# Kernel tuning notes

Measured on AMD Instinct MI355X. Metric: run time of the kernel, lower is better.

The kernel has to match this reference:

```python
import jax, jax.numpy as jnp
import numpy as np

INPUT_SIZE = 1024
NUM_QUBITS = 12
EMBED_SIZE = 2 ** NUM_QUBITS  # 4096
BATCH = 4096


def setup_inputs() -> dict:
    key = jax.random.key(0)
    k_x, k_w, k_p = jax.random.split(key, 3)
    x = jax.random.normal(k_x, (BATCH, INPUT_SIZE), dtype=jnp.float32)
    quantum_weights = jax.random.normal(k_w, (INPUT_SIZE, EMBED_SIZE), dtype=jnp.float32)
    quantum_phases = jax.random.normal(k_p, (INPUT_SIZE, NUM_QUBITS), dtype=jnp.float32)
    return {"x": x, "quantum_weights": quantum_weights, "quantum_phases": quantum_phases}


def reference(x, quantum_weights, quantum_phases):
    # Original: out[b] = Re( sum_j exp(i * mean(phases[j]) * x[b,j]) * W[j,:] ).
    # W is real, so the real part is sum_j cos(mean(phases[j]) * x[b,j]) * W[j,:],
    # i.e. a cosine-modulated matmul.
    phase_mean = jnp.mean(quantum_phases, axis=1)          # [input_size]
    coef = jnp.cos(x * phase_mean[None, :])                # [batch, input_size]
    return coef @ quantum_weights                          # [batch, embed_size]
```

## Files before the change

kernel.cpp:

```cpp
#include <hip/hip_runtime.h>
#include <hip/hip_bf16.h>


#define K_DIM 1024
#define N_DIM 4096
#define B_DIM 4096
#define NQ 12

typedef __attribute__((ext_vector_type(8))) _Float16 f16x8;
typedef __attribute__((ext_vector_type(4))) float f32x4;


__global__ void pm_kernel(const float* __restrict__ phases, float* __restrict__ pm) {
    int j = blockIdx.x * 256 + threadIdx.x;
    if (j < K_DIM) {
        float s = 0.f;
#pragma unroll
        for (int q = 0; q < NQ; ++q) s += phases[j * NQ + q];
        pm[j] = s * (1.0f / NQ);
    }
}

__global__ void asplit_kernel(const float* __restrict__ x, const float* __restrict__ pm,
                              char* __restrict__ Ah) {
    int i = blockIdx.x * 256 + threadIdx.x;
    int row = i >> 7;
    int k0  = (i & 127) << 3;
    const float* xp = x + ((size_t)row << 10) + k0;
    float4 xa = *(const float4*)xp;
    float4 xb = *(const float4*)(xp + 4);
    float4 pa = *(const float4*)(pm + k0);
    float4 pb = *(const float4*)(pm + k0 + 4);
    f16x8 hv;
    hv[0] = (_Float16)__cosf(xa.x * pa.x); hv[1] = (_Float16)__cosf(xa.y * pa.y);
    hv[2] = (_Float16)__cosf(xa.z * pa.z); hv[3] = (_Float16)__cosf(xa.w * pa.w);
    hv[4] = (_Float16)__cosf(xb.x * pb.x); hv[5] = (_Float16)__cosf(xb.y * pb.y);
    hv[6] = (_Float16)__cosf(xb.z * pb.z); hv[7] = (_Float16)__cosf(xb.w * pb.w);
    int tm = row >> 8, kt = k0 >> 5;
    int r = row & 255, kk = k0 & 31;
    size_t base = ((size_t)tm * 32 + (size_t)kt) * 16384;
    int addr = ((r << 6) + (kk << 1)) ^ ((r & 7) << 4);
    *(f16x8*)(Ah + base + addr) = hv;
}

__global__ void wsplit_kernel(const float* __restrict__ W, char* __restrict__ Bf) {
    __shared__ float t[64][65];
    int n0 = blockIdx.x * 64, k0 = blockIdx.y * 64;
    int tid = threadIdx.x;
#pragma unroll
    for (int p = 0; p < 16; ++p) {
        int lin = p * 256 + tid;
        int kk = lin >> 6, nn = lin & 63;
        t[kk][nn] = W[(size_t)(k0 + kk) * N_DIM + n0 + nn];
    }
    __syncthreads();
    int tn = n0 >> 8;
#pragma unroll
    for (int p2 = 0; p2 < 2; ++p2) {
        int w = p2 * 256 + tid;
        int nn = w >> 3, oct = w & 7;
        int r = (n0 & 255) + nn;
        int kt = (k0 >> 5) + (oct >> 2);
        int kk = (oct & 3) * 8;
        f16x8 hv;
#pragma unroll
        for (int j = 0; j < 8; ++j) hv[j] = (_Float16)t[oct * 8 + j][nn];
        size_t base = ((size_t)tn * 32 + (size_t)kt) * 16384;
        int addr = ((r << 6) + (kk << 1)) ^ ((r & 7) << 4);
        *(f16x8*)(Bf + base + addr) = hv;
    }
}

#define GLL16(g, l)                                                           \
    __builtin_amdgcn_global_load_lds(                                         \
        (const __attribute__((address_space(1))) void*)(g),                   \
        (__attribute__((address_space(3))) void*)(l), 16, 0, 0)

__global__ __launch_bounds__(512, 2) void gemm_kernel(
        const char* __restrict__ Ah, const char* __restrict__ Bf,
        float* __restrict__ C) {
    __shared__ char lds[98304];
    const int tid  = threadIdx.x;
    const int lane = tid & 63;
    const int wid  = tid >> 6;
    const int wm = wid >> 2, wn = wid & 3;
    const int fr   = lane & 15;
    const int colb = (lane >> 4) << 4;

    int wg  = blockIdx.x;
    int swz = (wg & 7) * 32 + (wg >> 3);
    int by = swz >> 4, bx = swz & 15;

    const char* pA = Ah + (size_t)by * 32 * 16384;
    const char* pB = Bf + (size_t)bx * 32 * 16384;

    int aAddr[8], bAddr[4];
#pragma unroll
    for (int m = 0; m < 8; ++m) {
        int r = wm * 128 + m * 16 + fr;
        aAddr[m] = ((r << 6) + colb) ^ ((r & 7) << 4);
    }
#pragma unroll
    for (int n = 0; n < 4; ++n) {
        int r = wn * 64 + n * 16 + fr;
        bAddr[n] = ((r << 6) + colb) ^ ((r & 7) << 4);
    }

    const int so = tid << 4;

#pragma unroll
    for (int t = 0; t < 2; ++t) {
        char* d = lds + t * 32768;
        const char* sA = pA + t * 16384;
        const char* sB = pB + t * 16384;
        GLL16(sA + so, d + so);
        GLL16(sA + 8192 + so, d + 8192 + so);
        GLL16(sB + so, d + 16384 + so);
        GLL16(sB + 8192 + so, d + 24576 + so);
    }

    f32x4 acc[8][4];
#pragma unroll
    for (int m = 0; m < 8; ++m)
#pragma unroll
        for (int n = 0; n < 4; ++n)
            acc[m][n] = (f32x4){0.f, 0.f, 0.f, 0.f};

    for (int t = 0; t < 32; ++t) {
        asm volatile("s_waitcnt vmcnt(4)" ::: "memory");
        __builtin_amdgcn_s_barrier();
        __builtin_amdgcn_sched_barrier(0);

        int t2 = (t + 2) & 31;
        char* d2 = lds + ((t + 2) % 3) * 32768;
        const char* sA = pA + t2 * 16384;
        const char* sB = pB + t2 * 16384;
        GLL16(sA + so, d2 + so);
        GLL16(sA + 8192 + so, d2 + 8192 + so);
        GLL16(sB + so, d2 + 16384 + so);
        GLL16(sB + 8192 + so, d2 + 24576 + so);

        const char* bufA = lds + (t % 3) * 32768;
        const char* bufB = bufA + 16384;
        f16x8 aH[8], bF[4];
#pragma unroll
        for (int m = 0; m < 8; ++m) aH[m] = *(const f16x8*)(bufA + aAddr[m]);
#pragma unroll
        for (int n = 0; n < 4; ++n) bF[n] = *(const f16x8*)(bufB + bAddr[n]);

        __builtin_amdgcn_s_setprio(1);
#pragma unroll
        for (int m = 0; m < 8; ++m)
#pragma unroll
            for (int n = 0; n < 4; ++n)
                acc[m][n] = __builtin_amdgcn_mfma_f32_16x16x32_f16(aH[m], bF[n], acc[m][n], 0, 0, 0);
        __builtin_amdgcn_s_setprio(0);
    }

    const int crow0 = by * 256 + wm * 128 + ((lane >> 4) << 2);
    const int ccol0 = bx * 256 + wn * 64 + fr;
#pragma unroll
    for (int m = 0; m < 8; ++m)
#pragma unroll
        for (int n = 0; n < 4; ++n) {
            size_t base = (size_t)(crow0 + m * 16) * N_DIM + (size_t)(ccol0 + n * 16);
#pragma unroll
            for (int j = 0; j < 4; ++j)
                C[base + (size_t)j * N_DIM] = acc[m][n][j];
        }
}

extern "C" void kernel_launch(void* const* d_in, const int* in_sizes, int n_in,
                              void* d_out, int out_size, void* d_ws, size_t ws_size,
                              hipStream_t stream) {
    const float* x      = (const float*)d_in[0];
    const float* W      = (const float*)d_in[1];
    const float* phases = (const float*)d_in[2];
    float* out = (float*)d_out;

    char* ws = (char*)d_ws;
    float* pm = (float*)ws;
    char* Ah = ws + 65536;
    char* Bf = Ah + (size_t)8 * 1024 * 1024;

    pm_kernel<<<4, 256, 0, stream>>>(phases, pm);
    asplit_kernel<<<(B_DIM * (K_DIM / 8)) / 256, 256, 0, stream>>>(x, pm, Ah);
    wsplit_kernel<<<dim3(N_DIM / 64, K_DIM / 64), 256, 0, stream>>>(W, Bf);
    gemm_kernel<<<256, 512, 0, stream>>>(Ah, Bf, out);
}
```

Baseline: 135.1 us.

## Switch GEMM to 64-deep K tiles with interleaved double-buffered loads

Repacks the fp16 A and B operands into 32 KB tiles holding 64 K-values each, two 32-wide halves per tile. The GEMM main loop now runs 16 iterations over a 128 KB LDS double buffer instead of 32 iterations over a 96 KB triple buffer. Async global-to-LDS loads for the next tile are split into four chunks and interleaved with the MFMA sub-blocks of the current tile. The goal is fewer loop iterations and better overlap of memory traffic with matrix math, in exchange for more barriers per iteration and higher LDS use per block.

Result: faster. 131.9 us (-2.4%).

```diff
diff --git a/kernel.cpp b/kernel.cpp
--- a/kernel.cpp
+++ b/kernel.cpp
@@ -36,9 +36,9 @@
     hv[2] = (_Float16)__cosf(xa.z * pa.z); hv[3] = (_Float16)__cosf(xa.w * pa.w);
     hv[4] = (_Float16)__cosf(xb.x * pb.x); hv[5] = (_Float16)__cosf(xb.y * pb.y);
     hv[6] = (_Float16)__cosf(xb.z * pb.z); hv[7] = (_Float16)__cosf(xb.w * pb.w);
-    int tm = row >> 8, kt = k0 >> 5;
+    int tr = row >> 8, kt = k0 >> 6, khalf = (k0 & 63) >> 5;
     int r = row & 255, kk = k0 & 31;
-    size_t base = ((size_t)tm * 32 + (size_t)kt) * 16384;
+    size_t base = ((size_t)tr * 16 + (size_t)kt) * 32768 + (size_t)khalf * 16384;
     int addr = ((r << 6) + (kk << 1)) ^ ((r & 7) << 4);
     *(f16x8*)(Ah + base + addr) = hv;
 }
@@ -54,20 +54,20 @@
         t[kk][nn] = W[(size_t)(k0 + kk) * N_DIM + n0 + nn];
     }
     __syncthreads();
-    int tn = n0 >> 8;
+    int tr = n0 >> 8, kt = k0 >> 6;
+    size_t tbase = ((size_t)tr * 16 + (size_t)kt) * 32768;
 #pragma unroll
     for (int p2 = 0; p2 < 2; ++p2) {
         int w = p2 * 256 + tid;
         int nn = w >> 3, oct = w & 7;
         int r = (n0 & 255) + nn;
-        int kt = (k0 >> 5) + (oct >> 2);
+        int khalf = oct >> 2;
         int kk = (oct & 3) * 8;
         f16x8 hv;
 #pragma unroll
         for (int j = 0; j < 8; ++j) hv[j] = (_Float16)t[oct * 8 + j][nn];
-        size_t base = ((size_t)tn * 32 + (size_t)kt) * 16384;
         int addr = ((r << 6) + (kk << 1)) ^ ((r & 7) << 4);
-        *(f16x8*)(Bf + base + addr) = hv;
+        *(f16x8*)(Bf + tbase + (size_t)khalf * 16384 + addr) = hv;
     }
 }
 
@@ -79,7 +79,7 @@
 __global__ __launch_bounds__(512, 2) void gemm_kernel(
         const char* __restrict__ Ah, const char* __restrict__ Bf,
         float* __restrict__ C) {
-    __shared__ char lds[98304];
+    __shared__ char lds[131072];
     const int tid  = threadIdx.x;
     const int lane = tid & 63;
     const int wid  = tid >> 6;
@@ -89,35 +89,34 @@
 
     int wg  = blockIdx.x;
     int swz = (wg & 7) * 32 + (wg >> 3);
-    int by = swz >> 4, bx = swz & 15;
-
-    const char* pA = Ah + (size_t)by * 32 * 16384;
-    const char* pB = Bf + (size_t)bx * 32 * 16384;
-
-    int aAddr[8], bAddr[4];
+    const int by = swz >> 4, bx = swz & 15;
+
+    const char* pA = Ah + (size_t)by * 16 * 32768;
+    const char* pB = Bf + (size_t)bx * 16 * 32768;
+
+    int aOff[8], bOff[4];
 #pragma unroll
     for (int m = 0; m < 8; ++m) {
         int r = wm * 128 + m * 16 + fr;
-        aAddr[m] = ((r << 6) + colb) ^ ((r & 7) << 4);
+        aOff[m] = ((r << 6) + colb) ^ ((r & 7) << 4);
     }
 #pragma unroll
     for (int n = 0; n < 4; ++n) {
         int r = wn * 64 + n * 16 + fr;
-        bAddr[n] = ((r << 6) + colb) ^ ((r & 7) << 4);
+        bOff[n] = ((r << 6) + colb) ^ ((r & 7) << 4);
     }
 
     const int so = tid << 4;
 
 #pragma unroll
-    for (int t = 0; t < 2; ++t) {
-        char* d = lds + t * 32768;
-        const char* sA = pA + t * 16384;
-        const char* sB = pB + t * 16384;
-        GLL16(sA + so, d + so);
-        GLL16(sA + 8192 + so, d + 8192 + so);
-        GLL16(sB + so, d + 16384 + so);
-        GLL16(sB + 8192 + so, d + 24576 + so);
-    }
+    for (int c = 0; c < 4; ++c) {
+        const char* s = ((c & 1) ? pB : pA) + (c >> 1) * 16384;
+        char* d = lds + c * 16384;
+        GLL16(s + so, d + so);
+        GLL16(s + 8192 + so, d + 8192 + so);
+    }
+    asm volatile("s_waitcnt vmcnt(4)" ::: "memory");
+    __builtin_amdgcn_s_barrier();
 
     f32x4 acc[8][4];
 #pragma unroll
@@ -126,35 +125,53 @@
         for (int n = 0; n < 4; ++n)
             acc[m][n] = (f32x4){0.f, 0.f, 0.f, 0.f};
 
-    for (int t = 0; t < 32; ++t) {
-        asm volatile("s_waitcnt vmcnt(4)" ::: "memory");
-        __builtin_amdgcn_s_barrier();
-        __builtin_amdgcn_sched_barrier(0);
-
-        int t2 = (t + 2) & 31;
-        char* d2 = lds + ((t + 2) % 3) * 32768;
-        const char* sA = pA + t2 * 16384;
-        const char* sB = pB + t2 * 16384;
-        GLL16(sA + so, d2 + so);
-        GLL16(sA + 8192 + so, d2 + 8192 + so);
-        GLL16(sB + so, d2 + 16384 + so);
-        GLL16(sB + 8192 + so, d2 + 24576 + so);
-
-        const char* bufA = lds + (t % 3) * 32768;
-        const char* bufB = bufA + 16384;
-        f16x8 aH[8], bF[4];
-#pragma unroll
-        for (int m = 0; m < 8; ++m) aH[m] = *(const f16x8*)(bufA + aAddr[m]);
-#pragma unroll
-        for (int n = 0; n < 4; ++n) bF[n] = *(const f16x8*)(bufB + bAddr[n]);
-
-        __builtin_amdgcn_s_setprio(1);
-#pragma unroll
-        for (int m = 0; m < 8; ++m)
-#pragma unroll
-            for (int n = 0; n < 4; ++n)
-                acc[m][n] = __builtin_amdgcn_mfma_f32_16x16x32_f16(aH[m], bF[n], acc[m][n], 0, 0, 0);
-        __builtin_amdgcn_s_setprio(0);
+    for (int t = 0; t < 16; ++t) {
+        const int cur = t & 1;
+        const char* bufc = lds + cur * 65536;
+        char* bufn = lds + (cur ^ 1) * 65536;
+        const char* srcA = pA + (size_t)((t + 1) & 15) * 32768;
+        const char* srcB = pB + (size_t)((t + 1) & 15) * 32768;
+
+#pragma unroll
+        for (int kh = 0; kh < 2; ++kh) {
+            f16x8 bF[4];
+#pragma unroll
+            for (int mh = 0; mh < 2; ++mh) {
+                if (mh == 0) {
+#pragma unroll
+                    for (int n = 0; n < 4; ++n)
+                        bF[n] = *(const f16x8*)(bufc + 16384 + kh * 32768 + bOff[n]);
+                }
+                f16x8 aH[4];
+#pragma unroll
+                for (int q = 0; q < 4; ++q)
+                    aH[q] = *(const f16x8*)(bufc + kh * 32768 + aOff[mh * 4 + q]);
+
+                {
+                    const int c = kh * 2 + mh;
+                    const char* s = ((c & 1) ? srcB : srcA) + (c >> 1) * 16384;
+                    char* d = bufn + c * 16384;
+                    GLL16(s + so, d + so);
+                    GLL16(s + 8192 + so, d + 8192 + so);
+                }
+
+                if (mh == 1)
+                    asm volatile("s_waitcnt vmcnt(4)" ::: "memory");
+
+                __builtin_amdgcn_s_barrier();
+
+                __builtin_amdgcn_s_setprio(1);
+#pragma unroll
+                for (int q = 0; q < 4; ++q)
+#pragma unroll
+                    for (int n = 0; n < 4; ++n)
+                        acc[mh * 4 + q][n] = __builtin_amdgcn_mfma_f32_16x16x32_f16(
+                            aH[q], bF[n], acc[mh * 4 + q][n], 0, 0, 0);
+                __builtin_amdgcn_s_setprio(0);
+
+                __builtin_amdgcn_s_barrier();
+            }
+        }
     }
 
     const int crow0 = by * 256 + wm * 128 + ((lane >> 4) << 2);
```
